# Optimization experiments

Measured on AMD Instinct MI355X. Metric: run time of the kernel, lower is better.

## Reference

```python
import jax, jax.numpy as jnp
import numpy as np

H = 1024       # hidden_size
I = 1024       # intermediate_size
E = 16         # num_experts
K = 4          # experts_per_token
LIMIT = 7.0    # swiglu_limit
ALPHA = 1.702  # swiglu alpha
EPS = 1e-5     # rmsnorm eps


def setup_inputs() -> dict:
    key = jax.random.key(0)
    ks = jax.random.split(key, 8)
    x = jax.random.normal(ks[0], (2, 512, H), dtype=jnp.float32)
    norm_scale = jnp.ones((H,), dtype=jnp.float32)
    wg = jax.random.normal(ks[1], (H, E), dtype=jnp.float32) * 0.02
    bg = jax.random.normal(ks[2], (E,), dtype=jnp.float32) * 0.02
    w1 = jax.random.normal(ks[3], (E, H, 2 * I), dtype=jnp.float32) * 0.02
    b1 = jax.random.normal(ks[4], (E, 2 * I), dtype=jnp.float32) * 0.02
    w2 = jax.random.normal(ks[5], (E, I, H), dtype=jnp.float32) * 0.02
    b2 = jax.random.normal(ks[6], (E, H), dtype=jnp.float32) * 0.02
    return {"x": x, "norm_scale": norm_scale, "wg": wg, "bg": bg,
            "w1": w1, "b1": b1, "w2": w2, "b2": b2}


def reference(x, norm_scale, wg, bg, w1, b1, w2, b2):
    shape = x.shape
    xf = x.reshape(-1, shape[-1])                                   # [T, H]
    # RMSNorm (float32 math)
    xn = xf * jax.lax.rsqrt(jnp.mean(xf * xf, axis=-1, keepdims=True) + EPS) * norm_scale
    # router logits + top-k with softmax over selected logits
    logits = xn @ wg + bg                                           # [T, E]
    vals, idx = jax.lax.top_k(logits, K)                            # [T, K]
    gates = jax.nn.softmax(vals, axis=-1)                           # [T, K]
    # dense [T, E] gate matrix (exactly equivalent to gather/scatter grouped GEMM)
    gate_full = jnp.einsum('tke,tk->te', jax.nn.one_hot(idx, E, dtype=gates.dtype), gates)
    # expert FFN 1 + fused swiglu (interleaved gate/linear pairs)
    h = jnp.einsum('th,ehd->etd', xn, w1) + b1[:, None, :]          # [E, T, 2I]
    a = jnp.minimum(h[..., ::2], LIMIT)                             # gate branch
    b = jnp.clip(h[..., 1::2], -LIMIT, LIMIT)                       # linear branch
    s = a * jax.nn.sigmoid(ALPHA * a) * (b + 1.0)                   # [E, T, I]
    # expert FFN 2; gamma (gate) scales the full epilogue incl. bias
    y = jnp.einsum('eti,eih->eth', s, w2) + b2[:, None, :]          # [E, T, H]
    t = jnp.einsum('eth,te->th', y, gate_full)                      # scatter-combine
    return x + t.reshape(shape)
```

## Files before the change

kernel.cpp:

```cpp
#include <hip/hip_runtime.h>

#define NH 1024
#define NI2 2048
#define NI 1024
#define NE 16
#define NT 1024

static constexpr float LIMITF = 7.0f;
static constexpr float ALPHAF = 1.702f;
static constexpr float EPSF = 1e-5f;

typedef short bf16x8 __attribute__((ext_vector_type(8)));
typedef float f32x16 __attribute__((ext_vector_type(16)));

__device__ __forceinline__ unsigned short f2bf(float f) {
  unsigned int u = __builtin_bit_cast(unsigned int, f);
  u = (u + 0x7FFFu + ((u >> 16) & 1u)) >> 16;
  return (unsigned short)u;
}

__global__ __launch_bounds__(256) void k_init(const float* __restrict__ x,
                                              float* __restrict__ out) {
  int i = blockIdx.x * 256 + threadIdx.x;
  reinterpret_cast<float4*>(out)[i] = reinterpret_cast<const float4*>(x)[i];
}

__global__ __launch_bounds__(256) void k_norm_router(
    const float* __restrict__ x, const float* __restrict__ nsc,
    const float* __restrict__ wg, const float* __restrict__ bg,
    unsigned short* __restrict__ xn, int* __restrict__ topk_idx,
    float* __restrict__ topk_gate, int* __restrict__ counts) {
  int t = blockIdx.x;
  int tid = threadIdx.x;
  int wave = tid >> 6, lane = tid & 63;

  float4 v = reinterpret_cast<const float4*>(x + (size_t)t * NH)[tid];
  float ss = v.x * v.x + v.y * v.y + v.z * v.z + v.w * v.w;
  for (int off = 32; off; off >>= 1) ss += __shfl_xor(ss, off);

  __shared__ float red[4];
  __shared__ float redl[4][16];
  __shared__ float logits_s[16];
  if (lane == 0) red[wave] = ss;
  __syncthreads();
  float tot = red[0] + red[1] + red[2] + red[3];
  float r = rsqrtf(tot * (1.0f / NH) + EPSF);

  float4 sc = reinterpret_cast<const float4*>(nsc)[tid];
  float xv[4];
  xv[0] = v.x * r * sc.x;
  xv[1] = v.y * r * sc.y;
  xv[2] = v.z * r * sc.z;
  xv[3] = v.w * r * sc.w;

  ushort4 o;
  o.x = f2bf(xv[0]); o.y = f2bf(xv[1]); o.z = f2bf(xv[2]); o.w = f2bf(xv[3]);
  reinterpret_cast<ushort4*>(xn + (size_t)t * NH)[tid] = o;

  float acc[16];
#pragma unroll
  for (int e = 0; e < 16; e++) acc[e] = 0.f;
  int hbase = tid * 4;
#pragma unroll
  for (int i = 0; i < 4; i++) {
    const float4* wr = reinterpret_cast<const float4*>(wg + (size_t)(hbase + i) * NE);
#pragma unroll
    for (int j = 0; j < 4; j++) {
      float4 w = wr[j];
      acc[j * 4 + 0] += xv[i] * w.x;
      acc[j * 4 + 1] += xv[i] * w.y;
      acc[j * 4 + 2] += xv[i] * w.z;
      acc[j * 4 + 3] += xv[i] * w.w;
    }
  }
#pragma unroll
  for (int e = 0; e < 16; e++)
    for (int off = 32; off; off >>= 1) acc[e] += __shfl_xor(acc[e], off);
  if (lane == 0) {
#pragma unroll
    for (int e = 0; e < 16; e++) redl[wave][e] = acc[e];
  }
  __syncthreads();
  if (tid < 16)
    logits_s[tid] = redl[0][tid] + redl[1][tid] + redl[2][tid] + redl[3][tid] + bg[tid];
  __syncthreads();

  if (tid == 0) {
    float vals[16];
#pragma unroll
    for (int e = 0; e < 16; e++) vals[e] = logits_s[e];
    int sel[4]; float sv[4];
    unsigned used = 0;
    for (int k = 0; k < 4; k++) {
      float best = -1e30f; int bi = 0;
      for (int e = 0; e < 16; e++) {
        if (!((used >> e) & 1u) && vals[e] > best) { best = vals[e]; bi = e; }
      }
      used |= 1u << bi; sel[k] = bi; sv[k] = best;
    }
    float g[4], ssum = 0.f;
    for (int k = 0; k < 4; k++) { g[k] = __expf(sv[k] - sv[0]); ssum += g[k]; }
    for (int k = 0; k < 4; k++) {
      topk_idx[t * 4 + k] = sel[k];
      topk_gate[t * 4 + k] = g[k] / ssum;
      atomicAdd(&counts[sel[k]], 1);
    }
  }
}

__global__ void k_scan(const int* __restrict__ counts, int* __restrict__ offsets,
                       int* __restrict__ cursor) {
  if (blockIdx.x == 0 && threadIdx.x == 0) {
    int o = 0;
    for (int e = 0; e < NE; e++) { offsets[e] = o; cursor[e] = o; o += counts[e]; }
  }
}

__global__ __launch_bounds__(256) void k_fill(const int* __restrict__ topk_idx,
                                              const float* __restrict__ topk_gate,
                                              int* __restrict__ cursor,
                                              int* __restrict__ rows_tok,
                                              float* __restrict__ rows_gate) {
  int idx = blockIdx.x * 256 + threadIdx.x;
  if (idx >= NT * 4) return;
  int e = topk_idx[idx];
  int slot = atomicAdd(&cursor[e], 1);
  rows_tok[slot] = idx >> 2;
  rows_gate[slot] = topk_gate[idx];
}

__global__ __launch_bounds__(256) void k_ffn1(
    const unsigned short* __restrict__ xn, const float* __restrict__ w1,
    const float* __restrict__ b1, const int* __restrict__ counts,
    const int* __restrict__ offsets, const int* __restrict__ rows_tok,
    unsigned short* __restrict__ s_buf) {
  int e = blockIdx.y;
  int cnt = counts[e];
  if (cnt == 0) return;
  int n0 = blockIdx.x * 32;
  int rowbase = offsets[e];
  int tid = threadIdx.x;

  __shared__ __align__(16) unsigned short lds_b[128 * 32 * 8];

  const float* w1e = w1 + (size_t)e * (NH * NI2) + n0;
  {
    int col = tid & 31;
    int kc8 = tid >> 5;
    for (int p = 0; p < 16; p++) {
      int kb = p * 64 + kc8 * 8;
      float f[8];
#pragma unroll
      for (int j = 0; j < 8; j++) f[j] = w1e[(size_t)(kb + j) * NI2 + col];
      unsigned int pk[4];
#pragma unroll
      for (int j = 0; j < 4; j++)
        pk[j] = (unsigned)f2bf(f[2 * j]) | ((unsigned)f2bf(f[2 * j + 1]) << 16);
      *reinterpret_cast<uint4*>(&lds_b[(size_t)((kb >> 3) * 32 + col) * 8]) =
          *reinterpret_cast<const uint4*>(pk);
    }
  }
  __syncthreads();

  int lane = tid & 63;
  int wave = tid >> 6;
  int lrow = lane & 31;
  int khalf = lane >> 5;

  float bias = b1[(size_t)e * NI2 + n0 + lrow];
  int parity = lrow & 1;

  for (int m0 = 0; m0 < cnt; m0 += 256) {
    int tb0 = m0 + wave * 32;
    int tb1 = m0 + 128 + wave * 32;
    int tok0 = rows_tok[rowbase + min(tb0 + lrow, cnt - 1)];
    const unsigned short* a0p = xn + (size_t)tok0 * NH + khalf * 8;

    f32x16 acc0 = {0.f,0.f,0.f,0.f,0.f,0.f,0.f,0.f,0.f,0.f,0.f,0.f,0.f,0.f,0.f,0.f};
    f32x16 acc1 = {0.f,0.f,0.f,0.f,0.f,0.f,0.f,0.f,0.f,0.f,0.f,0.f,0.f,0.f,0.f,0.f};
    bool dual = (m0 + 128) < cnt;

    if (dual) {
      int tok1 = rows_tok[rowbase + min(tb1 + lrow, cnt - 1)];
      const unsigned short* a1p = xn + (size_t)tok1 * NH + khalf * 8;
#pragma unroll 4
      for (int k2 = 0; k2 < 64; k2++) {
        bf16x8 av0 = *reinterpret_cast<const bf16x8*>(a0p + k2 * 16);
        bf16x8 av1 = *reinterpret_cast<const bf16x8*>(a1p + k2 * 16);
        bf16x8 bv = *reinterpret_cast<const bf16x8*>(
            &lds_b[(size_t)((k2 * 2 + khalf) * 32 + lrow) * 8]);
        acc0 = __builtin_amdgcn_mfma_f32_32x32x16_bf16(av0, bv, acc0, 0, 0, 0);
        acc1 = __builtin_amdgcn_mfma_f32_32x32x16_bf16(av1, bv, acc1, 0, 0, 0);
      }
    } else {
#pragma unroll 4
      for (int k2 = 0; k2 < 64; k2++) {
        bf16x8 av0 = *reinterpret_cast<const bf16x8*>(a0p + k2 * 16);
        bf16x8 bv = *reinterpret_cast<const bf16x8*>(
            &lds_b[(size_t)((k2 * 2 + khalf) * 32 + lrow) * 8]);
        acc0 = __builtin_amdgcn_mfma_f32_32x32x16_bf16(av0, bv, acc0, 0, 0, 0);
      }
    }

#pragma unroll
    for (int t2 = 0; t2 < 2; t2++) {
      if (t2 == 1 && !dual) break;
      f32x16 acc = t2 ? acc1 : acc0;
      int tb = t2 ? tb1 : tb0;
#pragma unroll
      for (int reg = 0; reg < 16; reg++) {
        float v = acc[reg] + bias;
        float p = __shfl_xor(v, 1);
        int row = (reg & 3) + 8 * (reg >> 2) + 4 * khalf;
        int m = tb + row;
        if (!parity && m < cnt) {
          float aa = fminf(v, LIMITF);
          float bb = fminf(fmaxf(p, -LIMITF), LIMITF);
          float sig = 1.0f / (1.0f + __expf(-ALPHAF * aa));
          float sval = aa * sig * (bb + 1.0f);
          s_buf[(size_t)(rowbase + m) * NI + ((n0 + lrow) >> 1)] = f2bf(sval);
        }
      }
    }
  }
}

__global__ __launch_bounds__(256) void k_ffn2(
    const unsigned short* __restrict__ s_buf, const float* __restrict__ w2,
    const float* __restrict__ b2, const int* __restrict__ counts,
    const int* __restrict__ offsets, const int* __restrict__ rows_tok,
    const float* __restrict__ rows_gate, float* __restrict__ out) {
  int e = blockIdx.y;
  int cnt = counts[e];
  if (cnt == 0) return;
  int n0 = blockIdx.x * 32;
  int rowbase = offsets[e];
  int tid = threadIdx.x;

  __shared__ __align__(16) unsigned short lds_b[128 * 32 * 8];

  const float* w2e = w2 + (size_t)e * (NI * NH) + n0;
  {
    int col = tid & 31;
    int kc8 = tid >> 5;
    for (int p = 0; p < 16; p++) {
      int kb = p * 64 + kc8 * 8;
      float f[8];
#pragma unroll
      for (int j = 0; j < 8; j++) f[j] = w2e[(size_t)(kb + j) * NH + col];
      unsigned int pk[4];
#pragma unroll
      for (int j = 0; j < 4; j++)
        pk[j] = (unsigned)f2bf(f[2 * j]) | ((unsigned)f2bf(f[2 * j + 1]) << 16);
      *reinterpret_cast<uint4*>(&lds_b[(size_t)((kb >> 3) * 32 + col) * 8]) =
          *reinterpret_cast<const uint4*>(pk);
    }
  }
  __syncthreads();

  int lane = tid & 63;
  int wave = tid >> 6;
  int lrow = lane & 31;
  int khalf = lane >> 5;

  float b2v = b2[(size_t)e * NH + n0 + lrow];

  for (int m0 = 0; m0 < cnt; m0 += 256) {
    int tb0 = m0 + wave * 32;
    int tb1 = m0 + 128 + wave * 32;
    int r0 = rowbase + min(tb0 + lrow, cnt - 1);
    const unsigned short* a0p = s_buf + (size_t)r0 * NI + khalf * 8;

    f32x16 acc0 = {0.f,0.f,0.f,0.f,0.f,0.f,0.f,0.f,0.f,0.f,0.f,0.f,0.f,0.f,0.f,0.f};
    f32x16 acc1 = {0.f,0.f,0.f,0.f,0.f,0.f,0.f,0.f,0.f,0.f,0.f,0.f,0.f,0.f,0.f,0.f};
    bool dual = (m0 + 128) < cnt;

    if (dual) {
      int r1 = rowbase + min(tb1 + lrow, cnt - 1);
      const unsigned short* a1p = s_buf + (size_t)r1 * NI + khalf * 8;
#pragma unroll 4
      for (int k2 = 0; k2 < 64; k2++) {
        bf16x8 av0 = *reinterpret_cast<const bf16x8*>(a0p + k2 * 16);
        bf16x8 av1 = *reinterpret_cast<const bf16x8*>(a1p + k2 * 16);
        bf16x8 bv = *reinterpret_cast<const bf16x8*>(
            &lds_b[(size_t)((k2 * 2 + khalf) * 32 + lrow) * 8]);
        acc0 = __builtin_amdgcn_mfma_f32_32x32x16_bf16(av0, bv, acc0, 0, 0, 0);
        acc1 = __builtin_amdgcn_mfma_f32_32x32x16_bf16(av1, bv, acc1, 0, 0, 0);
      }
    } else {
#pragma unroll 4
      for (int k2 = 0; k2 < 64; k2++) {
        bf16x8 av0 = *reinterpret_cast<const bf16x8*>(a0p + k2 * 16);
        bf16x8 bv = *reinterpret_cast<const bf16x8*>(
            &lds_b[(size_t)((k2 * 2 + khalf) * 32 + lrow) * 8]);
        acc0 = __builtin_amdgcn_mfma_f32_32x32x16_bf16(av0, bv, acc0, 0, 0, 0);
      }
    }

#pragma unroll
    for (int t2 = 0; t2 < 2; t2++) {
      if (t2 == 1 && !dual) break;
      f32x16 acc = t2 ? acc1 : acc0;
      int tb = t2 ? tb1 : tb0;
#pragma unroll
      for (int reg = 0; reg < 16; reg++) {
        int row = (reg & 3) + 8 * (reg >> 2) + 4 * khalf;
        int m = tb + row;
        if (m < cnt) {
          int rr = rowbase + m;
          int tok = rows_tok[rr];
          float g = rows_gate[rr];
          atomicAdd(&out[(size_t)tok * NH + n0 + lrow], g * (acc[reg] + b2v));
        }
      }
    }
  }
}

extern "C" void kernel_launch(void* const* d_in, const int* in_sizes, int n_in,
                              void* d_out, int out_size, void* d_ws, size_t ws_size,
                              hipStream_t stream) {
  const float* x   = (const float*)d_in[0];
  const float* nsc = (const float*)d_in[1];
  const float* wg  = (const float*)d_in[2];
  const float* bg  = (const float*)d_in[3];
  const float* w1  = (const float*)d_in[4];
  const float* b1  = (const float*)d_in[5];
  const float* w2  = (const float*)d_in[6];
  const float* b2  = (const float*)d_in[7];
  float* out = (float*)d_out;
  char* ws = (char*)d_ws;

  int*   counts    = (int*)(ws + 0);
  int*   offsets   = (int*)(ws + 64);
  int*   cursor    = (int*)(ws + 128);
  int*   topk_idx  = (int*)(ws + 1024);
  float* topk_gate = (float*)(ws + 1024 + 16384);
  int*   rows_tok  = (int*)(ws + 1024 + 32768);
  float* rows_gate = (float*)(ws + 1024 + 49152);
  unsigned short* xn    = (unsigned short*)(ws + 131072);
  unsigned short* s_buf = (unsigned short*)(ws + 4 * 1024 * 1024);

  hipMemsetAsync(ws, 0, 256, stream);
  k_init<<<NT * NH / 1024, 256, 0, stream>>>(x, out);
  k_norm_router<<<NT, 256, 0, stream>>>(x, nsc, wg, bg, xn, topk_idx, topk_gate,
                                        counts);
  k_scan<<<1, 64, 0, stream>>>(counts, offsets, cursor);
  k_fill<<<16, 256, 0, stream>>>(topk_idx, topk_gate, cursor, rows_tok, rows_gate);
  k_ffn1<<<dim3(NI2 / 32, NE), 256, 0, stream>>>(xn, w1, b1, counts, offsets,
                                                 rows_tok, s_buf);
  k_ffn2<<<dim3(NH / 32, NE), 256, 0, stream>>>(s_buf, w2, b2, counts, offsets,
                                                rows_tok, rows_gate, out);
}
```

Baseline: 453.3 us.

## Gather routed tokens into MFMA-tiled layout and store swiglu output tiled

Adds a gather kernel that copies each expert's routed token rows into a 32-row tiled layout padded to 32-row groups, so FFN1 reads A operands contiguously instead of through an indirect, strided per-token gather. FFN1 writes its swiglu output in the same tiled layout so FFN2's A loads also become coalesced 512-byte chunks. Expert offsets are padded to multiples of 32 to keep groups aligned. This costs an extra kernel launch and an extra pass over the activations, and the tiled writes of s are scattered 2-byte stores.

```diff
diff --git a/kernel.cpp b/kernel.cpp
--- a/kernel.cpp
+++ b/kernel.cpp
@@ -112,7 +112,10 @@
                        int* __restrict__ cursor) {
   if (blockIdx.x == 0 && threadIdx.x == 0) {
     int o = 0;
-    for (int e = 0; e < NE; e++) { offsets[e] = o; cursor[e] = o; o += counts[e]; }
+    for (int e = 0; e < NE; e++) {
+      offsets[e] = o; cursor[e] = o;
+      o += (counts[e] + 31) & ~31;
+    }
   }
 }
 
@@ -129,11 +132,32 @@
   rows_gate[slot] = topk_gate[idx];
 }
 
+__global__ __launch_bounds__(256) void k_gather(
+    const unsigned short* __restrict__ xn, const int* __restrict__ counts,
+    const int* __restrict__ offsets, const int* __restrict__ rows_tok,
+    unsigned short* __restrict__ xg) {
+  int e = blockIdx.y;
+  int g = blockIdx.x;
+  int cnt = counts[e];
+  if (g * 32 >= cnt) return;
+  int tid = threadIdx.x;
+  int r = tid & 31, kq = tid >> 5;
+  int rowbase = offsets[e];
+  int tok = rows_tok[rowbase + min(g * 32 + r, cnt - 1)];
+  const uint4* src = reinterpret_cast<const uint4*>(xn + (size_t)tok * NH);
+  uint4* dst = reinterpret_cast<uint4*>(
+      xg + ((size_t)(rowbase >> 5) + g) * (128 * 32 * 8));
+#pragma unroll
+  for (int i = 0; i < 16; i++) {
+    int ko = i * 8 + kq;
+    dst[ko * 32 + r] = src[ko];
+  }
+}
+
 __global__ __launch_bounds__(256) void k_ffn1(
-    const unsigned short* __restrict__ xn, const float* __restrict__ w1,
+    const unsigned short* __restrict__ xg, const float* __restrict__ w1,
     const float* __restrict__ b1, const int* __restrict__ counts,
-    const int* __restrict__ offsets, const int* __restrict__ rows_tok,
-    unsigned short* __restrict__ s_buf) {
+    const int* __restrict__ offsets, unsigned short* __restrict__ s_tiled) {
   int e = blockIdx.y;
   int cnt = counts[e];
   if (cnt == 0) return;
@@ -173,20 +197,20 @@
   for (int m0 = 0; m0 < cnt; m0 += 256) {
     int tb0 = m0 + wave * 32;
     int tb1 = m0 + 128 + wave * 32;
-    int tok0 = rows_tok[rowbase + min(tb0 + lrow, cnt - 1)];
-    const unsigned short* a0p = xn + (size_t)tok0 * NH + khalf * 8;
+    const unsigned short* a0p =
+        xg + ((size_t)((rowbase + tb0) >> 5) * 128 + khalf) * 256 + lrow * 8;
 
     f32x16 acc0 = {0.f,0.f,0.f,0.f,0.f,0.f,0.f,0.f,0.f,0.f,0.f,0.f,0.f,0.f,0.f,0.f};
     f32x16 acc1 = {0.f,0.f,0.f,0.f,0.f,0.f,0.f,0.f,0.f,0.f,0.f,0.f,0.f,0.f,0.f,0.f};
     bool dual = (m0 + 128) < cnt;
 
     if (dual) {
-      int tok1 = rows_tok[rowbase + min(tb1 + lrow, cnt - 1)];
-      const unsigned short* a1p = xn + (size_t)tok1 * NH + khalf * 8;
+      const unsigned short* a1p =
+          xg + ((size_t)((rowbase + tb1) >> 5) * 128 + khalf) * 256 + lrow * 8;
 #pragma unroll 4
       for (int k2 = 0; k2 < 64; k2++) {
-        bf16x8 av0 = *reinterpret_cast<const bf16x8*>(a0p + k2 * 16);
-        bf16x8 av1 = *reinterpret_cast<const bf16x8*>(a1p + k2 * 16);
+        bf16x8 av0 = *reinterpret_cast<const bf16x8*>(a0p + k2 * 512);
+        bf16x8 av1 = *reinterpret_cast<const bf16x8*>(a1p + k2 * 512);
         bf16x8 bv = *reinterpret_cast<const bf16x8*>(
             &lds_b[(size_t)((k2 * 2 + khalf) * 32 + lrow) * 8]);
         acc0 = __builtin_amdgcn_mfma_f32_32x32x16_bf16(av0, bv, acc0, 0, 0, 0);
@@ -195,7 +219,7 @@
     } else {
 #pragma unroll 4
       for (int k2 = 0; k2 < 64; k2++) {
-        bf16x8 av0 = *reinterpret_cast<const bf16x8*>(a0p + k2 * 16);
+        bf16x8 av0 = *reinterpret_cast<const bf16x8*>(a0p + k2 * 512);
         bf16x8 bv = *reinterpret_cast<const bf16x8*>(
             &lds_b[(size_t)((k2 * 2 + khalf) * 32 + lrow) * 8]);
         acc0 = __builtin_amdgcn_mfma_f32_32x32x16_bf16(av0, bv, acc0, 0, 0, 0);
@@ -218,7 +242,9 @@
           float bb = fminf(fmaxf(p, -LIMITF), LIMITF);
           float sig = 1.0f / (1.0f + __expf(-ALPHAF * aa));
           float sval = aa * sig * (bb + 1.0f);
-          s_buf[(size_t)(rowbase + m) * NI + ((n0 + lrow) >> 1)] = f2bf(sval);
+          int c = (n0 + lrow) >> 1;
+          size_t grp = (size_t)(rowbase + tb) >> 5;
+          s_tiled[(grp * 128 + (c >> 3)) * 256 + row * 8 + (c & 7)] = f2bf(sval);
         }
       }
     }
@@ -226,7 +252,7 @@
 }
 
 __global__ __launch_bounds__(256) void k_ffn2(
-    const unsigned short* __restrict__ s_buf, const float* __restrict__ w2,
+    const unsigned short* __restrict__ s_tiled, const float* __restrict__ w2,
     const float* __restrict__ b2, const int* __restrict__ counts,
     const int* __restrict__ offsets, const int* __restrict__ rows_tok,
     const float* __restrict__ rows_gate, float* __restrict__ out) {
@@ -268,20 +294,20 @@
   for (int m0 = 0; m0 < cnt; m0 += 256) {
     int tb0 = m0 + wave * 32;
     int tb1 = m0 + 128 + wave * 32;
-    int r0 = rowbase + min(tb0 + lrow, cnt - 1);
-    const unsigned short* a0p = s_buf + (size_t)r0 * NI + khalf * 8;
+    const unsigned short* a0p =
+        s_tiled + ((size_t)((rowbase + tb0) >> 5) * 128 + khalf) * 256 + lrow * 8;
 
     f32x16 acc0 = {0.f,0.f,0.f,0.f,0.f,0.f,0.f,0.f,0.f,0.f,0.f,0.f,0.f,0.f,0.f,0.f};
     f32x16 acc1 = {0.f,0.f,0.f,0.f,0.f,0.f,0.f,0.f,0.f,0.f,0.f,0.f,0.f,0.f,0.f,0.f};
     bool dual = (m0 + 128) < cnt;
 
     if (dual) {
-      int r1 = rowbase + min(tb1 + lrow, cnt - 1);
-      const unsigned short* a1p = s_buf + (size_t)r1 * NI + khalf * 8;
+      const unsigned short* a1p =
+          s_tiled + ((size_t)((rowbase + tb1) >> 5) * 128 + khalf) * 256 + lrow * 8;
 #pragma unroll 4
       for (int k2 = 0; k2 < 64; k2++) {
-        bf16x8 av0 = *reinterpret_cast<const bf16x8*>(a0p + k2 * 16);
-        bf16x8 av1 = *reinterpret_cast<const bf16x8*>(a1p + k2 * 16);
+        bf16x8 av0 = *reinterpret_cast<const bf16x8*>(a0p + k2 * 512);
+        bf16x8 av1 = *reinterpret_cast<const bf16x8*>(a1p + k2 * 512);
         bf16x8 bv = *reinterpret_cast<const bf16x8*>(
             &lds_b[(size_t)((k2 * 2 + khalf) * 32 + lrow) * 8]);
         acc0 = __builtin_amdgcn_mfma_f32_32x32x16_bf16(av0, bv, acc0, 0, 0, 0);
@@ -290,7 +316,7 @@
     } else {
 #pragma unroll 4
       for (int k2 = 0; k2 < 64; k2++) {
-        bf16x8 av0 = *reinterpret_cast<const bf16x8*>(a0p + k2 * 16);
+        bf16x8 av0 = *reinterpret_cast<const bf16x8*>(a0p + k2 * 512);
         bf16x8 bv = *reinterpret_cast<const bf16x8*>(
             &lds_b[(size_t)((k2 * 2 + khalf) * 32 + lrow) * 8]);
         acc0 = __builtin_amdgcn_mfma_f32_32x32x16_bf16(av0, bv, acc0, 0, 0, 0);
@@ -335,11 +361,12 @@
   int*   offsets   = (int*)(ws + 64);
   int*   cursor    = (int*)(ws + 128);
   int*   topk_idx  = (int*)(ws + 1024);
-  float* topk_gate = (float*)(ws + 1024 + 16384);
-  int*   rows_tok  = (int*)(ws + 1024 + 32768);
-  float* rows_gate = (float*)(ws + 1024 + 49152);
-  unsigned short* xn    = (unsigned short*)(ws + 131072);
-  unsigned short* s_buf = (unsigned short*)(ws + 4 * 1024 * 1024);
+  float* topk_gate = (float*)(ws + 17408);
+  int*   rows_tok  = (int*)(ws + 33792);
+  float* rows_gate = (float*)(ws + 54272);
+  unsigned short* xn      = (unsigned short*)(ws + 131072);
+  unsigned short* xg      = (unsigned short*)(ws + 2228224);
+  unsigned short* s_tiled = (unsigned short*)(ws + 12 * 1024 * 1024);
 
   hipMemsetAsync(ws, 0, 256, stream);
   k_init<<<NT * NH / 1024, 256, 0, stream>>>(x, out);
@@ -347,8 +374,9 @@
                                         counts);
   k_scan<<<1, 64, 0, stream>>>(counts, offsets, cursor);
   k_fill<<<16, 256, 0, stream>>>(topk_idx, topk_gate, cursor, rows_tok, rows_gate);
-  k_ffn1<<<dim3(NI2 / 32, NE), 256, 0, stream>>>(xn, w1, b1, counts, offsets,
-                                                 rows_tok, s_buf);
-  k_ffn2<<<dim3(NH / 32, NE), 256, 0, stream>>>(s_buf, w2, b2, counts, offsets,
+  k_gather<<<dim3(128, NE), 256, 0, stream>>>(xn, counts, offsets, rows_tok, xg);
+  k_ffn1<<<dim3(NI2 / 32, NE), 256, 0, stream>>>(xg, w1, b1, counts, offsets,
+                                                 s_tiled);
+  k_ffn2<<<dim3(NH / 32, NE), 256, 0, stream>>>(s_tiled, w2, b2, counts, offsets,
                                                 rows_tok, rows_gate, out);
 }
```

New measurement: 441.1 us. 2.7% less time.
